# Kernel tuning notes

Hardware: AMD Instinct MI355X
Metric: run time of the kernel (lower is better)

## Reference

```python
import jax, jax.numpy as jnp
import numpy as np

N = 30000      # particles
E = 300000     # directed edges
H = 128        # hidden size
L = 10         # GNN layers
EMB = 16       # particle-type embedding size
T = 5          # velocity history window
NTYPES = 9
RADIUS = 0.05
OUT = 2
NODE_IN = 2 * T + 4 + EMB  # 30


def _mlp_ln(x, W1, b1, W2, b2, W3, b3, g, be):
    # Linear-ReLU-Linear-ReLU-Linear-LayerNorm (matches node/edge encoders and GraphNet blocks)
    h = jax.nn.relu(x @ W1 + b1)
    h = jax.nn.relu(h @ W2 + b2)
    h = h @ W3 + b3
    mu = jnp.mean(h, axis=-1, keepdims=True)
    var = jnp.mean((h - mu) ** 2, axis=-1, keepdims=True)
    return (h - mu) * jax.lax.rsqrt(var + 1e-5) * g + be


def setup_inputs() -> dict:
    key = jax.random.key(0)
    ks = iter(jax.random.split(key, 48))
    nx = lambda: next(ks)
    inp = {}
    inp["vel"] = jax.random.normal(nx(), (N, T, 2), jnp.float32) * 0.01
    inp["pos"] = jax.random.uniform(nx(), (N, 2), dtype=jnp.float32)
    inp["bounds"] = jnp.array([[0.0, 1.0], [0.0, 1.0]], jnp.float32)  # [dim, (lo,hi)]
    inp["tgt_pos"] = jax.random.uniform(nx(), (N, 2), dtype=jnp.float32)
    inp["particle_type"] = jax.random.randint(nx(), (N,), 0, NTYPES, jnp.int32)
    inp["nonk_mask"] = jax.random.randint(nx(), (N,), 0, 2, jnp.int32)
    inp["senders"] = jax.random.randint(nx(), (E,), 0, N, jnp.int32)
    inp["receivers"] = jax.random.randint(nx(), (E,), 0, N, jnp.int32)
    inp["emb"] = jax.random.normal(nx(), (NTYPES, EMB), jnp.float32) * 0.1

    def mlp_p(pre, din, lead=()):
        w = lambda i, o: jax.random.normal(nx(), lead + (i, o), jnp.float32) / np.sqrt(i)
        inp[pre + "_W1"] = w(din, H); inp[pre + "_b1"] = jnp.zeros(lead + (H,), jnp.float32)
        inp[pre + "_W2"] = w(H, H);   inp[pre + "_b2"] = jnp.zeros(lead + (H,), jnp.float32)
        inp[pre + "_W3"] = w(H, H);   inp[pre + "_b3"] = jnp.zeros(lead + (H,), jnp.float32)
        inp[pre + "_g"] = jnp.ones(lead + (H,), jnp.float32)
        inp[pre + "_be"] = jnp.zeros(lead + (H,), jnp.float32)

    mlp_p("ne", NODE_IN)          # node encoder
    mlp_p("ee", 3)                # edge encoder
    mlp_p("ge", 3 * H, (L,))      # per-layer edge-update MLPs
    mlp_p("gn", 2 * H, (L,))      # per-layer node-update MLPs
    inp["de_W1"] = jax.random.normal(nx(), (H, H), jnp.float32) / np.sqrt(H)
    inp["de_b1"] = jnp.zeros((H,), jnp.float32)
    inp["de_W2"] = jax.random.normal(nx(), (H, H), jnp.float32) / np.sqrt(H)
    inp["de_b2"] = jnp.zeros((H,), jnp.float32)
    inp["de_W3"] = jax.random.normal(nx(), (H, OUT), jnp.float32) / np.sqrt(H)
    inp["de_b3"] = jnp.zeros((OUT,), jnp.float32)
    return inp


def reference(vel, pos, bounds, tgt_pos, particle_type, nonk_mask, senders, receivers, emb,
              ne_W1, ne_b1, ne_W2, ne_b2, ne_W3, ne_b3, ne_g, ne_be,
              ee_W1, ee_b1, ee_W2, ee_b2, ee_W3, ee_b3, ee_g, ee_be,
              ge_W1, ge_b1, ge_W2, ge_b2, ge_W3, ge_b3, ge_g, ge_be,
              gn_W1, gn_b1, gn_W2, gn_b2, gn_W3, gn_b3, gn_g, gn_be,
              de_W1, de_b1, de_W2, de_b2, de_W3, de_b3):
    n = pos.shape[0]
    # --- construct node features ---
    vels = vel.reshape(n, -1)                                   # [N, T*2]
    dtw = jnp.concatenate([pos - bounds[:, 0], bounds[:, 1] - pos], axis=1)
    dtw = jnp.clip(dtw / RADIUS, -1.0, 1.0)                     # [N, 4]
    type_emb = emb[particle_type]                               # [N, EMB] gather
    node_attr = jnp.concatenate([vels, dtw, type_emb], axis=1)  # [N, 30]
    # --- construct edge features (senders/receivers precomputed; KD-tree is CPU-side) ---
    dist_vec = (pos[senders] - pos[receivers]) / RADIUS         # [E, 2]
    dist = jnp.linalg.norm(dist_vec, axis=1, keepdims=True)     # [E, 1]
    edge_attr = jnp.concatenate([dist_vec, dist], axis=1)       # [E, 3]
    # --- encode ---
    nodes = _mlp_ln(node_attr, ne_W1, ne_b1, ne_W2, ne_b2, ne_W3, ne_b3, ne_g, ne_be)
    edges = _mlp_ln(edge_attr, ee_W1, ee_b1, ee_W2, ee_b2, ee_W3, ee_b3, ee_g, ee_be)
    # --- process: L message-passing layers with residuals ---
    for l in range(ge_W1.shape[0]):
        e_in = jnp.concatenate([edges, nodes[senders], nodes[receivers]], axis=1)  # [E, 3H]
        edges = edges + _mlp_ln(e_in, ge_W1[l], ge_b1[l], ge_W2[l], ge_b2[l], ge_W3[l], ge_b3[l], ge_g[l], ge_be[l])
        agg = jax.ops.segment_sum(edges, receivers, num_segments=n)               # [N, H] scatter-add
        n_in = jnp.concatenate([nodes, agg], axis=1)                              # [N, 2H]
        nodes = nodes + _mlp_ln(n_in, gn_W1[l], gn_b1[l], gn_W2[l], gn_b2[l], gn_W3[l], gn_b3[l], gn_g[l], gn_be[l])
    # --- decode ---
    h = jax.nn.relu(nodes @ de_W1 + de_b1)
    h = jax.nn.relu(h @ de_W2 + de_b2)
    pred_acc = h @ de_W3 + de_b3                                 # [N, 2]
    # --- Euler integration step (out_size == 2 branch) ---
    pred_pos = pos + vel[:, -1, :] + pred_acc
    pred_pos = jnp.where(nonk_mask[:, None].astype(bool), pred_pos, tgt_pos)
    return pred_acc[:, None, :], pred_pos[:, None, :]
```

## Files before the change

### kernel.cpp

```cpp
#include <hip/hip_runtime.h>
#include <hip/hip_bf16.h>

typedef __hip_bfloat16 bf16;
typedef unsigned short u16;
typedef unsigned int u32;
typedef __attribute__((ext_vector_type(8))) short short8;
typedef __attribute__((ext_vector_type(4))) float f32x4;

#define NPART 30000
#define NEDGE 300000
#define HD 128
#define NLAYER 10
#define NFLOAT_ARRAYS 43
#define NMAT 66

__device__ __forceinline__ bool detect_bf16(const unsigned short* braw) {
    return braw[1] == 0x3F80u;
}

__device__ __forceinline__ u16 f2b(float f) {
    u32 u = __float_as_uint(f);
    u += 0x7FFFu + ((u >> 16) & 1u);
    return (u16)(u >> 16);
}
__device__ __forceinline__ u32 pack2(float a, float b) {
    return (u32)f2b(a) | ((u32)f2b(b) << 16);
}
__device__ __forceinline__ float b2flo(u32 u) { return __uint_as_float(u << 16); }
__device__ __forceinline__ float b2fhi(u32 u) { return __uint_as_float(u & 0xFFFF0000u); }

struct ConvArgs {
    const void* src[NFLOAT_ARRAYS];
    int n[NFLOAT_ARRAYS];
    int off[NFLOAT_ARRAYS];
};

__global__ __launch_bounds__(256)
void k_convert(ConvArgs a, float* __restrict__ dst, const unsigned short* __restrict__ braw)
{
    const bool isb = detect_bf16(braw);
    const int aid = blockIdx.y;
    const int n = a.n[aid];
    float* o = dst + a.off[aid];
    const int stride = gridDim.x * 256;
    int i = blockIdx.x * 256 + threadIdx.x;
    if (isb) {
        const unsigned short* s = (const unsigned short*)a.src[aid];
        for (; i < n; i += stride) {
            const unsigned int u = ((unsigned int)s[i]) << 16;
            o[i] = __uint_as_float(u);
        }
    } else {
        const float* s = (const float*)a.src[aid];
        for (; i < n; i += stride) o[i] = s[i];
    }
}

__global__ __launch_bounds__(256)
void k_hist(const int* __restrict__ rcv, int* __restrict__ counts)
{
    const int e = blockIdx.x * 256 + threadIdx.x;
    if (e < NEDGE) atomicAdd(&counts[rcv[e]], 1);
}

__global__ __launch_bounds__(1024)
void k_scan(const int* __restrict__ counts, int* __restrict__ row_ptr, int* __restrict__ cursor)
{
    __shared__ int part[1024];
    const int t = threadIdx.x;
    const int base = t * 32;
    int local[32];
    int s = 0;
#pragma unroll
    for (int k = 0; k < 32; k++) {
        const int idx = base + k;
        const int v = (idx < NPART) ? counts[idx] : 0;
        local[k] = s;
        s += v;
    }
    part[t] = s;
    __syncthreads();
    for (int off = 1; off < 1024; off <<= 1) {
        const int v = (t >= off) ? part[t - off] : 0;
        __syncthreads();
        part[t] += v;
        __syncthreads();
    }
    const int excl = (t == 0) ? 0 : part[t - 1];
#pragma unroll
    for (int k = 0; k < 32; k++) {
        const int idx = base + k;
        if (idx < NPART) {
            const int rp = excl + local[k];
            row_ptr[idx] = rp;
            cursor[idx] = rp;
        }
    }
    if (t == 0) row_ptr[NPART] = NEDGE;
}

__global__ __launch_bounds__(256)
void k_scatter(const int* __restrict__ snd, const int* __restrict__ rcv,
               int* __restrict__ cursor, int* __restrict__ snd_s, int* __restrict__ rcv_s)
{
    const int e = blockIdx.x * 256 + threadIdx.x;
    if (e < NEDGE) {
        const int r = rcv[e];
        const int p = atomicAdd(&cursor[r], 1);
        snd_s[p] = snd[e];
        rcv_s[p] = r;
    }
}

struct PackArgs {
    int src_off[NMAT];
    int dst_off[NMAT];
    int K[NMAT];
    int nks[NMAT];
};

__global__ __launch_bounds__(256)
void k_pack(const float* __restrict__ cw, u16* __restrict__ wpk, PackArgs pa)
{
    const int mid = blockIdx.y;
    const int nks = pa.nks[mid];
    const int total = nks * 4096;
    const int d = blockIdx.x * 256 + threadIdx.x;
    if (d >= total) return;
    const int j = d & 7, l = (d >> 3) & 63, t = d >> 9;
    const int ks = t % nks, mt = t / nks;
    const int hid = mt * 16 + (l & 15);
    const int k = ks * 32 + (l >> 4) * 8 + j;
    const float v = (k < pa.K[mid]) ? cw[pa.src_off[mid] + k * HD + hid] : 0.0f;
    wpk[pa.dst_off[mid] + d] = f2b(v);
}

template<int NKS, int XROW>
__device__ __forceinline__ void gemm16(const u16* __restrict__ Wp,
                                       const float* __restrict__ Bias,
                                       const u16* __restrict__ x,
                                       f32x4 acc[4][2],
                                       const int wm, const int wn,
                                       const int l15, const int lg, const int lane)
{
#pragma unroll
    for (int mt = 0; mt < 4; mt++) {
        const f32x4 bv = *(const f32x4*)(Bias + wm * 64 + mt * 16 + lg * 4);
        acc[mt][0] = bv;
        acc[mt][1] = bv;
    }
    const u16* xr0 = x + (wn * 32 + l15) * XROW + lg * 8;
    const u16* xr1 = xr0 + 16 * XROW;
    const u16* wp = Wp + (wm * 4 * NKS) * 512 + lane * 8;
#pragma unroll
    for (int ks = 0; ks < NKS; ks++) {
        const short8 b0 = *(const short8*)(xr0 + ks * 32);
        const short8 b1 = *(const short8*)(xr1 + ks * 32);
#pragma unroll
        for (int mt = 0; mt < 4; mt++) {
            const short8 a = *(const short8*)(wp + (mt * NKS + ks) * 512);
            acc[mt][0] = __builtin_amdgcn_mfma_f32_16x16x32_bf16(a, b0, acc[mt][0], 0, 0, 0);
            acc[mt][1] = __builtin_amdgcn_mfma_f32_16x16x32_bf16(a, b1, acc[mt][1], 0, 0, 0);
        }
    }
}

__device__ __forceinline__ void store_h(u16* __restrict__ h, const f32x4 acc[4][2],
                                        const int wm, const int wn, const int l15, const int lg)
{
#pragma unroll
    for (int nt = 0; nt < 2; nt++) {
        const int e = wn * 32 + nt * 16 + l15;
#pragma unroll
        for (int mt = 0; mt < 4; mt++) {
            const int hid = wm * 64 + mt * 16 + lg * 4;
            const f32x4 v = acc[mt][nt];
            const u32 lo = pack2(fmaxf(v[0], 0.0f), fmaxf(v[1], 0.0f));
            const u32 hi = pack2(fmaxf(v[2], 0.0f), fmaxf(v[3], 0.0f));
            *(uint2*)(h + e * 136 + hid) = make_uint2(lo, hi);
        }
    }
}

template<int NKS1, int XROW>
__device__ __forceinline__ void mlp_mfma(const u16* __restrict__ xs,
    u16* __restrict__ h1, u16* __restrict__ h2,
    float (*red)[2][2][16][2],
    const u16* __restrict__ W1p, const float* __restrict__ B1,
    const u16* __restrict__ W2p, const float* __restrict__ B2,
    const u16* __restrict__ W3p, const float* __restrict__ B3,
    const float* __restrict__ g, const float* __restrict__ be,
    float outv[4][2][4],
    const int wm, const int wn, const int l15, const int lg, const int lane)
{
    f32x4 acc[4][2];
    gemm16<NKS1, XROW>(W1p, B1, xs, acc, wm, wn, l15, lg, lane);
    __syncthreads();
    store_h(h1, acc, wm, wn, l15, lg);
    __syncthreads();
    gemm16<4, 136>(W2p, B2, h1, acc, wm, wn, l15, lg, lane);
    store_h(h2, acc, wm, wn, l15, lg);
    __syncthreads();
    gemm16<4, 136>(W3p, B3, h2, acc, wm, wn, l15, lg, lane);
    float ps[2], pss[2];
#pragma unroll
    for (int nt = 0; nt < 2; nt++) {
        float s = 0.0f, ss = 0.0f;
#pragma unroll
        for (int mt = 0; mt < 4; mt++) {
#pragma unroll
            for (int r = 0; r < 4; r++) {
                const float v = acc[mt][nt][r];
                s += v; ss += v * v;
            }
        }
        s += __shfl_xor(s, 16); ss += __shfl_xor(ss, 16);
        s += __shfl_xor(s, 32); ss += __shfl_xor(ss, 32);
        ps[nt] = s; pss[nt] = ss;
    }
    if (lane < 16) {
#pragma unroll
        for (int nt = 0; nt < 2; nt++) {
            red[wm][wn][nt][l15][0] = ps[nt];
            red[wm][wn][nt][l15][1] = pss[nt];
        }
    }
    __syncthreads();
#pragma unroll
    for (int nt = 0; nt < 2; nt++) {
        const float S  = red[0][wn][nt][l15][0] + red[1][wn][nt][l15][0];
        const float SS = red[0][wn][nt][l15][1] + red[1][wn][nt][l15][1];
        const float mu  = S * (1.0f / 128.0f);
        const float var = SS * (1.0f / 128.0f) - mu * mu;
        const float inv = rsqrtf(var + 1e-5f);
#pragma unroll
        for (int mt = 0; mt < 4; mt++) {
            const int hid = wm * 64 + mt * 16 + lg * 4;
            const f32x4 gv  = *(const f32x4*)(g + hid);
            const f32x4 bev = *(const f32x4*)(be + hid);
#pragma unroll
            for (int r = 0; r < 4; r++)
                outv[mt][nt][r] = (acc[mt][nt][r] - mu) * inv * gv[r] + bev[r];
        }
    }
}

__device__ __forceinline__ float nfeat(int i, int k,
    const float* __restrict__ vel, const float* __restrict__ pos,
    const float* __restrict__ bounds, const int* __restrict__ ptype,
    const float* __restrict__ emb)
{
    if (k < 10) return vel[i * 10 + k];
    if (k < 14) {
        const int q = k - 10;
        float sub;
        if (q < 2) sub = pos[i * 2 + q] - bounds[q * 2 + 0];
        else       sub = bounds[(q - 2) * 2 + 1] - pos[i * 2 + (q - 2)];
        const float dv = sub * 20.0f;
        return fminf(fmaxf(dv, -1.0f), 1.0f);
    }
    if (k < 30) return emb[ptype[i] * 16 + (k - 14)];
    return 0.0f;
}

__global__ __launch_bounds__(256)
void k_node_enc_m(const float* __restrict__ vel, const float* __restrict__ pos,
                  const float* __restrict__ bounds, const int* __restrict__ ptype,
                  const float* __restrict__ emb,
                  const u16* __restrict__ W1p, const float* __restrict__ B1,
                  const u16* __restrict__ W2p, const float* __restrict__ B2,
                  const u16* __restrict__ W3p, const float* __restrict__ B3,
                  const float* __restrict__ g, const float* __restrict__ be,
                  float* __restrict__ nodes, u16* __restrict__ nodes_bf)
{
    __shared__ __align__(16) u16 lds[17408];
    __shared__ float red[2][2][2][16][2];
    const int tid = threadIdx.x;
    const int i0 = blockIdx.x * 64;
    for (int idx = tid; idx < 1024; idx += 256) {
        const int m = idx >> 4, kk = idx & 15;
        const int i = i0 + m;
        float f0 = 0.0f, f1 = 0.0f;
        if (i < NPART) {
            f0 = nfeat(i, kk * 2 + 0, vel, pos, bounds, ptype, emb);
            f1 = nfeat(i, kk * 2 + 1, vel, pos, bounds, ptype, emb);
        }
        *(u32*)(lds + m * 40 + kk * 2) = pack2(f0, f1);
    }
    __syncthreads();
    const int lane = tid & 63, wv = tid >> 6;
    const int wm = wv >> 1, wn = wv & 1, l15 = lane & 15, lg = lane >> 4;
    float outv[4][2][4];
    mlp_mfma<1, 40>(lds, lds, lds + 8704, red, W1p, B1, W2p, B2, W3p, B3, g, be,
                    outv, wm, wn, l15, lg, lane);
#pragma unroll
    for (int nt = 0; nt < 2; nt++) {
        const int i = i0 + wn * 32 + nt * 16 + l15;
        if (i < NPART) {
#pragma unroll
            for (int mt = 0; mt < 4; mt++) {
                const int hid = wm * 64 + mt * 16 + lg * 4;
                const float4 v = make_float4(outv[mt][nt][0], outv[mt][nt][1],
                                             outv[mt][nt][2], outv[mt][nt][3]);
                *(float4*)(nodes + (size_t)i * HD + hid) = v;
                *(uint2*)(nodes_bf + (size_t)i * HD + hid) =
                    make_uint2(pack2(v.x, v.y), pack2(v.z, v.w));
            }
        }
    }
}

__global__ __launch_bounds__(256)
void k_edge_enc_m(const float* __restrict__ pos, const int* __restrict__ snd_s,
                  const int* __restrict__ rcv_s,
                  const u16* __restrict__ W1p, const float* __restrict__ B1,
                  const u16* __restrict__ W2p, const float* __restrict__ B2,
                  const u16* __restrict__ W3p, const float* __restrict__ B3,
                  const float* __restrict__ g, const float* __restrict__ be,
                  u16* __restrict__ edges_bf)
{
    __shared__ __align__(16) u16 lds[17408];
    __shared__ float red[2][2][2][16][2];
    const int tid = threadIdx.x;
    const int e0 = blockIdx.x * 64;
    for (int idx = tid; idx < 1024; idx += 256) {
        const int m = idx >> 4, kk = idx & 15;
        const int e = min(e0 + m, NEDGE - 1);
        u32 w = 0;
        if (kk < 2) {
            const int s = snd_s[e], r = rcv_s[e];
            const float dx = (pos[s * 2 + 0] - pos[r * 2 + 0]) * 20.0f;
            const float dy = (pos[s * 2 + 1] - pos[r * 2 + 1]) * 20.0f;
            if (kk == 0) w = pack2(dx, dy);
            else         w = pack2(sqrtf(dx * dx + dy * dy), 0.0f);
        }
        *(u32*)(lds + m * 40 + kk * 2) = w;
    }
    __syncthreads();
    const int lane = tid & 63, wv = tid >> 6;
    const int wm = wv >> 1, wn = wv & 1, l15 = lane & 15, lg = lane >> 4;
    float outv[4][2][4];
    mlp_mfma<1, 40>(lds, lds, lds + 8704, red, W1p, B1, W2p, B2, W3p, B3, g, be,
                    outv, wm, wn, l15, lg, lane);
#pragma unroll
    for (int nt = 0; nt < 2; nt++) {
        const int e = e0 + wn * 32 + nt * 16 + l15;
        if (e < NEDGE) {
#pragma unroll
            for (int mt = 0; mt < 4; mt++) {
                const int hid = wm * 64 + mt * 16 + lg * 4;
                *(uint2*)(edges_bf + (size_t)e * HD + hid) =
                    make_uint2(pack2(outv[mt][nt][0], outv[mt][nt][1]),
                               pack2(outv[mt][nt][2], outv[mt][nt][3]));
            }
        }
    }
}

__device__ __forceinline__ void egemm_seg32(const u16* __restrict__ Wp,
                                            const u16* __restrict__ x,
                                            f32x4 acc[2][2], const int ks0,
                                            const int wm,
                                            const int l15, const int lg, const int lane)
{
    const u16* xr0 = x + l15 * 136 + lg * 8;
    const u16* xr1 = xr0 + 16 * 136;
#pragma unroll
    for (int ks = 0; ks < 4; ks++) {
        const short8 b0 = *(const short8*)(xr0 + ks * 32);
        const short8 b1 = *(const short8*)(xr1 + ks * 32);
#pragma unroll
        for (int mt = 0; mt < 2; mt++) {
            const short8 a = *(const short8*)(Wp + (((wm * 2 + mt) * 12 + ks0 + ks) * 64 + lane) * 8);
            acc[mt][0] = __builtin_amdgcn_mfma_f32_16x16x32_bf16(a, b0, acc[mt][0], 0, 0, 0);
            acc[mt][1] = __builtin_amdgcn_mfma_f32_16x16x32_bf16(a, b1, acc[mt][1], 0, 0, 0);
        }
    }
}

__device__ __forceinline__ void egemm_h32(const u16* __restrict__ Wp,
                                          const float* __restrict__ Bias,
                                          const u16* __restrict__ x,
                                          f32x4 acc[2][2],
                                          const int wm,
                                          const int l15, const int lg, const int lane)
{
#pragma unroll
    for (int mt = 0; mt < 2; mt++) {
        const f32x4 bv = *(const f32x4*)(Bias + wm * 32 + mt * 16 + lg * 4);
        acc[mt][0] = bv;
        acc[mt][1] = bv;
    }
    const u16* xr0 = x + l15 * 136 + lg * 8;
    const u16* xr1 = xr0 + 16 * 136;
#pragma unroll
    for (int ks = 0; ks < 4; ks++) {
        const short8 b0 = *(const short8*)(xr0 + ks * 32);
        const short8 b1 = *(const short8*)(xr1 + ks * 32);
#pragma unroll
        for (int mt = 0; mt < 2; mt++) {
            const short8 a = *(const short8*)(Wp + (((wm * 2 + mt) * 4 + ks) * 64 + lane) * 8);
            acc[mt][0] = __builtin_amdgcn_mfma_f32_16x16x32_bf16(a, b0, acc[mt][0], 0, 0, 0);
            acc[mt][1] = __builtin_amdgcn_mfma_f32_16x16x32_bf16(a, b1, acc[mt][1], 0, 0, 0);
        }
    }
}

__device__ __forceinline__ void estore_h32(u16* __restrict__ h, const f32x4 acc[2][2],
                                           const int wm, const int l15, const int lg)
{
#pragma unroll
    for (int nt = 0; nt < 2; nt++) {
        const int row = nt * 16 + l15;
#pragma unroll
        for (int mt = 0; mt < 2; mt++) {
            const int hid = wm * 32 + mt * 16 + lg * 4;
            const f32x4 v = acc[mt][nt];
            const u32 lo = pack2(fmaxf(v[0], 0.0f), fmaxf(v[1], 0.0f));
            const u32 hi = pack2(fmaxf(v[2], 0.0f), fmaxf(v[3], 0.0f));
            *(uint2*)(h + row * 136 + hid) = make_uint2(lo, hi);
        }
    }
}

__global__ __launch_bounds__(256, 8)
void k_edge_layer_m(const u16* __restrict__ nodes_bf, u16* __restrict__ edges_bf,
                    float* __restrict__ agg, float* __restrict__ bnd,
                    const int* __restrict__ snd_s, const int* __restrict__ rcv_s,
                    const u16* __restrict__ W1p, const float* __restrict__ B1,
                    const u16* __restrict__ W2p, const float* __restrict__ B2,
                    const u16* __restrict__ W3p, const float* __restrict__ B3,
                    const float* __restrict__ g, const float* __restrict__ be)
{
    __shared__ __align__(16) u16 sb[2 * 4352];
    __shared__ float red[4][2][16][2];
    __shared__ int rblk[34];
    u16* b0 = sb;
    u16* b1 = sb + 4352;
    float* fout = (float*)sb;

    const int tid = threadIdx.x;
    const int e0 = blockIdx.x * 32;
    const int lane = tid & 63, wm = tid >> 6;
    const int l15 = lane & 15, lg = lane >> 4;

    if (tid < 32)       rblk[tid] = rcv_s[e0 + tid];
    else if (tid == 32) rblk[32] = (e0 > 0) ? rcv_s[e0 - 1] : -2;
    else if (tid == 33) rblk[33] = (e0 + 32 < NEDGE) ? rcv_s[e0 + 32] : -2;

    uint4 e_old[2];
#pragma unroll
    for (int t = 0; t < 2; t++) {
        const int idx = tid + t * 256;
        const int m = idx >> 4, q = idx & 15;
        e_old[t] = *(const uint4*)(edges_bf + (size_t)(e0 + m) * HD + q * 8);
        *(uint4*)(b0 + m * 136 + q * 8) = e_old[t];
    }
    uint4 st[2];
#pragma unroll
    for (int t = 0; t < 2; t++) {
        const int idx = tid + t * 256;
        const int m = idx >> 4, q = idx & 15;
        st[t] = *(const uint4*)(nodes_bf + (size_t)snd_s[e0 + m] * HD + q * 8);
    }
    __syncthreads();

    f32x4 acc[2][2];
#pragma unroll
    for (int mt = 0; mt < 2; mt++) {
        const f32x4 bv = *(const f32x4*)(B1 + wm * 32 + mt * 16 + lg * 4);
        acc[mt][0] = bv;
        acc[mt][1] = bv;
    }
    __builtin_amdgcn_s_setprio(1);
    egemm_seg32(W1p, b0, acc, 0, wm, l15, lg, lane);
    __builtin_amdgcn_s_setprio(0);
#pragma unroll
    for (int t = 0; t < 2; t++) {
        const int idx = tid + t * 256;
        const int m = idx >> 4, q = idx & 15;
        *(uint4*)(b1 + m * 136 + q * 8) = st[t];
    }
#pragma unroll
    for (int t = 0; t < 2; t++) {
        const int idx = tid + t * 256;
        const int m = idx >> 4, q = idx & 15;
        st[t] = *(const uint4*)(nodes_bf + (size_t)rcv_s[e0 + m] * HD + q * 8);
    }
    __syncthreads();

    __builtin_amdgcn_s_setprio(1);
    egemm_seg32(W1p, b1, acc, 4, wm, l15, lg, lane);
    __builtin_amdgcn_s_setprio(0);
#pragma unroll
    for (int t = 0; t < 2; t++) {
        const int idx = tid + t * 256;
        const int m = idx >> 4, q = idx & 15;
        *(uint4*)(b0 + m * 136 + q * 8) = st[t];
    }
    __syncthreads();

    __builtin_amdgcn_s_setprio(1);
    egemm_seg32(W1p, b0, acc, 8, wm, l15, lg, lane);
    __builtin_amdgcn_s_setprio(0);
    estore_h32(b1, acc, wm, l15, lg);
    __syncthreads();

    __builtin_amdgcn_s_setprio(1);
    egemm_h32(W2p, B2, b1, acc, wm, l15, lg, lane);
    __builtin_amdgcn_s_setprio(0);
    estore_h32(b0, acc, wm, l15, lg);
    __syncthreads();

    __builtin_amdgcn_s_setprio(1);
    egemm_h32(W3p, B3, b0, acc, wm, l15, lg, lane);
    __builtin_amdgcn_s_setprio(0);

    float ps[2], pss[2];
#pragma unroll
    for (int nt = 0; nt < 2; nt++) {
        float s = 0.0f, ss = 0.0f;
#pragma unroll
        for (int mt = 0; mt < 2; mt++) {
#pragma unroll
            for (int r = 0; r < 4; r++) {
                const float v = acc[mt][nt][r];
                s += v; ss += v * v;
            }
        }
        s += __shfl_xor(s, 16); ss += __shfl_xor(ss, 16);
        s += __shfl_xor(s, 32); ss += __shfl_xor(ss, 32);
        ps[nt] = s; pss[nt] = ss;
    }
    if (lane < 16) {
#pragma unroll
        for (int nt = 0; nt < 2; nt++) {
            red[wm][nt][l15][0] = ps[nt];
            red[wm][nt][l15][1] = pss[nt];
        }
    }
    __syncthreads();

#pragma unroll
    for (int nt = 0; nt < 2; nt++) {
        const float S  = red[0][nt][l15][0] + red[1][nt][l15][0]
                       + red[2][nt][l15][0] + red[3][nt][l15][0];
        const float SS = red[0][nt][l15][1] + red[1][nt][l15][1]
                       + red[2][nt][l15][1] + red[3][nt][l15][1];
        const float mu  = S * (1.0f / 128.0f);
        const float var = SS * (1.0f / 128.0f) - mu * mu;
        const float inv = rsqrtf(var + 1e-5f);
        const int row = nt * 16 + l15;
#pragma unroll
        for (int mt = 0; mt < 2; mt++) {
            const int hid = wm * 32 + mt * 16 + lg * 4;
            const f32x4 gv  = *(const f32x4*)(g + hid);
            const f32x4 bev = *(const f32x4*)(be + hid);
            f32x4 o;
#pragma unroll
            for (int r = 0; r < 4; r++)
                o[r] = (acc[mt][nt][r] - mu) * inv * gv[r] + bev[r];
            *(f32x4*)(fout + row * 132 + hid) = o;
        }
    }
    __syncthreads();

#pragma unroll
    for (int t = 0; t < 2; t++) {
        const int idx = tid + t * 256;
        const int m = idx >> 4, q = idx & 15;
        float4 lo = *(const float4*)(fout + m * 132 + q * 8);
        float4 hi = *(const float4*)(fout + m * 132 + q * 8 + 4);
        const uint4 o = e_old[t];
        lo.x += b2flo(o.x); lo.y += b2fhi(o.x);
        lo.z += b2flo(o.y); lo.w += b2fhi(o.y);
        hi.x += b2flo(o.z); hi.y += b2fhi(o.z);
        hi.z += b2flo(o.w); hi.w += b2fhi(o.w);
        *(float4*)(fout + m * 132 + q * 8) = lo;
        *(float4*)(fout + m * 132 + q * 8 + 4) = hi;
        *(uint4*)(edges_bf + (size_t)(e0 + m) * HD + q * 8) =
            make_uint4(pack2(lo.x, lo.y), pack2(lo.z, lo.w),
                       pack2(hi.x, hi.y), pack2(hi.z, hi.w));
    }
    __syncthreads();

    const int c = tid & 31;
    for (int ms = (tid >> 5); ms < 32; ms += 8) {
        const int rs = rblk[ms];
        if (ms > 0 && rblk[ms - 1] == rs) continue;
        int me = ms + 1;
        while (me < 32 && rblk[me] == rs) me++;
        float4 s = make_float4(0.0f, 0.0f, 0.0f, 0.0f);
        for (int m = ms; m < me; m++) {
            const float4 v = *(const float4*)(fout + m * 132 + c * 4);
            s.x += v.x; s.y += v.y; s.z += v.z; s.w += v.w;
        }
        const bool extb = (ms == 0 && rblk[32] == rs);
        const bool extf = (me == 32 && rblk[33] == rs);
        float* ap;
        if (!extb && !extf) ap = agg + (size_t)rs * HD + c * 4;
        else ap = bnd + ((size_t)blockIdx.x * 2 + (extb ? 0 : 1)) * HD + c * 4;
        *(float4*)ap = s;
    }
}

__global__ __launch_bounds__(256)
void k_node_layer_m(float* __restrict__ nodes, u16* __restrict__ nodes_bf,
                    const float* __restrict__ agg, const float* __restrict__ bnd,
                    const int* __restrict__ row_ptr,
                    const u16* __restrict__ W1p, const float* __restrict__ B1,
                    const u16* __restrict__ W2p, const float* __restrict__ B2,
                    const u16* __restrict__ W3p, const float* __restrict__ B3,
                    const float* __restrict__ g, const float* __restrict__ be)
{
    __shared__ __align__(16) u16 lds[17408];
    __shared__ float red[2][2][2][16][2];
    __shared__ int rp[65];
    const int tid = threadIdx.x;
    const int i0 = blockIdx.x * 64;
    if (tid < 65) rp[tid] = row_ptr[min(i0 + tid, NPART)];
    __syncthreads();
    for (int idx = tid; idx < 1024; idx += 256) {
        const int m = idx >> 4, q = idx & 15;
        const int i = min(i0 + m, NPART - 1);
        const float* src = nodes + (size_t)i * HD + q * 8;
        const float4 a = *(const float4*)(src);
        const float4 b = *(const float4*)(src + 4);
        *(uint4*)(lds + m * 264 + q * 8) =
            make_uint4(pack2(a.x, a.y), pack2(a.z, a.w), pack2(b.x, b.y), pack2(b.z, b.w));
    }
    for (int idx = tid; idx < 1024; idx += 256) {
        const int m = idx >> 4, q = idx & 15;
        const int i = i0 + m;
        float4 a = make_float4(0.0f, 0.0f, 0.0f, 0.0f);
        float4 b = make_float4(0.0f, 0.0f, 0.0f, 0.0f);
        if (i < NPART) {
            const int p0 = rp[m], p1 = rp[m + 1];
            if (p1 > p0) {
                const int b0 = p0 >> 5, b1 = (p1 - 1) >> 5;
                if (b0 == b1) {
                    const float* src = agg + (size_t)i * HD + q * 8;
                    a = *(const float4*)(src);
                    b = *(const float4*)(src + 4);
                } else {
                    const float* s1 = bnd + ((size_t)b0 * 2 + 1) * HD + q * 8;
                    a = *(const float4*)(s1);
                    b = *(const float4*)(s1 + 4);
                    for (int bb = b0 + 1; bb <= b1; bb++) {
                        const float* s0 = bnd + ((size_t)bb * 2 + 0) * HD + q * 8;
                        const float4 xa = *(const float4*)(s0);
                        const float4 xb = *(const float4*)(s0 + 4);
                        a.x += xa.x; a.y += xa.y; a.z += xa.z; a.w += xa.w;
                        b.x += xb.x; b.y += xb.y; b.z += xb.z; b.w += xb.w;
                    }
                }
            }
        }
        *(uint4*)(lds + m * 264 + 128 + q * 8) =
            make_uint4(pack2(a.x, a.y), pack2(a.z, a.w), pack2(b.x, b.y), pack2(b.z, b.w));
    }
    __syncthreads();
    const int lane = tid & 63, wv = tid >> 6;
    const int wm = wv >> 1, wn = wv & 1, l15 = lane & 15, lg = lane >> 4;
    float outv[4][2][4];
    mlp_mfma<8, 264>(lds, lds, lds + 8704, red, W1p, B1, W2p, B2, W3p, B3, g, be,
                     outv, wm, wn, l15, lg, lane);
#pragma unroll
    for (int nt = 0; nt < 2; nt++) {
        const int i = i0 + wn * 32 + nt * 16 + l15;
        if (i < NPART) {
            float* np = nodes + (size_t)i * HD;
#pragma unroll
            for (int mt = 0; mt < 4; mt++) {
                const int hid = wm * 64 + mt * 16 + lg * 4;
                const float4 old = *(const float4*)(np + hid);
                const float4 nv = make_float4(old.x + outv[mt][nt][0],
                                              old.y + outv[mt][nt][1],
                                              old.z + outv[mt][nt][2],
                                              old.w + outv[mt][nt][3]);
                *(float4*)(np + hid) = nv;
                *(uint2*)(nodes_bf + (size_t)i * HD + hid) =
                    make_uint2(pack2(nv.x, nv.y), pack2(nv.z, nv.w));
            }
        }
    }
}

template<int K, int S>
__device__ __forceinline__ void gemv(const float* __restrict__ in,
                                     const float* __restrict__ W,
                                     const float* __restrict__ B,
                                     float acc[8])
{
    const int j = threadIdx.x;
    const float bb = B[j];
#pragma unroll
    for (int m = 0; m < 8; m++) acc[m] = bb;
    constexpr int K4 = (K / 4) * 4;
    for (int k = 0; k < K4; k += 4) {
        const float w0 = W[(k + 0) * HD + j];
        const float w1 = W[(k + 1) * HD + j];
        const float w2 = W[(k + 2) * HD + j];
        const float w3 = W[(k + 3) * HD + j];
#pragma unroll
        for (int m = 0; m < 8; m++) {
            const float4 x = *(const float4*)(in + m * S + k);
            float a = acc[m];
            a = fmaf(x.x, w0, a);
            a = fmaf(x.y, w1, a);
            a = fmaf(x.z, w2, a);
            a = fmaf(x.w, w3, a);
            acc[m] = a;
        }
    }
#pragma unroll
    for (int k = K4; k < K; k++) {
        const float w = W[k * HD + j];
#pragma unroll
        for (int m = 0; m < 8; m++) acc[m] = fmaf(in[m * S + k], w, acc[m]);
    }
}

__global__ __launch_bounds__(128)
void k_decoder(const float* __restrict__ nodes,
               const float* W1, const float* B1, const float* W2, const float* B2,
               const float* W3, const float* B3,
               const float* __restrict__ vel, const float* __restrict__ pos,
               const float* __restrict__ tgt, const int* __restrict__ nonk,
               const unsigned short* __restrict__ braw, void* __restrict__ d_out)
{
    __shared__ __align__(16) float xs[8 * HD];
    __shared__ __align__(16) float h1[8 * HD];
    __shared__ __align__(16) float h2[8 * HD];
    const int j = threadIdx.x;
    const int i0 = blockIdx.x * 8;
    float acc[8];
#pragma unroll
    for (int m = 0; m < 8; m++) xs[m * HD + j] = nodes[(i0 + m) * HD + j];
    __syncthreads();
    gemv<HD, HD>(xs, W1, B1, acc);
#pragma unroll
    for (int m = 0; m < 8; m++) h1[m * HD + j] = fmaxf(acc[m], 0.0f);
    __syncthreads();
    gemv<HD, HD>(h1, W2, B2, acc);
#pragma unroll
    for (int m = 0; m < 8; m++) h2[m * HD + j] = fmaxf(acc[m], 0.0f);
    __syncthreads();
    if (j < 16) {
        const int m = j >> 1, d = j & 1, i = i0 + m;
        float a = B3[d];
        for (int k = 0; k < HD; k++) a = fmaf(h2[m * HD + k], W3[k * 2 + d], a);
        float pp = pos[i * 2 + d] + vel[i * 10 + 8 + d] + a;
        if (nonk[i] == 0) pp = tgt[i * 2 + d];
        if (detect_bf16(braw)) {
            bf16* o = (bf16*)d_out;
            o[i * 2 + d] = __float2bfloat16(a);
            o[2 * NPART + i * 2 + d] = __float2bfloat16(pp);
        } else {
            float* o = (float*)d_out;
            o[i * 2 + d] = a;
            o[2 * NPART + i * 2 + d] = pp;
        }
    }
}

extern "C" void kernel_launch(void* const* d_in, const int* in_sizes, int n_in,
                              void* d_out, int out_size, void* d_ws, size_t ws_size,
                              hipStream_t stream)
{
    const int* ptype = (const int*)d_in[4];
    const int* nonk  = (const int*)d_in[5];
    const int* snd   = (const int*)d_in[6];
    const int* rcv   = (const int*)d_in[7];
    const unsigned short* braw = (const unsigned short*)d_in[2];

    int fmap[NFLOAT_ARRAYS];
    {
        int c = 0;
        fmap[c++] = 0; fmap[c++] = 1; fmap[c++] = 2; fmap[c++] = 3; fmap[c++] = 8;
        for (int i = 9; i <= 46; i++) fmap[c++] = i;
    }
    ConvArgs ca;
    const float* fp[47];
    float* cw = (float*)d_ws;
    int off = 0;
    for (int i = 0; i < NFLOAT_ARRAYS; i++) {
        ca.src[i] = d_in[fmap[i]];
        ca.n[i]   = in_sizes[fmap[i]];
        ca.off[i] = off;
        fp[fmap[i]] = cw + off;
        off += in_sizes[fmap[i]];
    }
    const int EB32 = NEDGE / 32;
    float* nodes = cw + ((off + 3) & ~3);
    float* agg   = nodes + (size_t)NPART * HD;
    float* bnd   = agg + (size_t)NPART * HD;
    u16* edges_bf = (u16*)(bnd + (size_t)EB32 * 2 * HD);
    u16* nodes_bf = edges_bf + (size_t)NEDGE * HD;
    u16* wpk = nodes_bf + (size_t)NPART * HD;

    PackArgs pa;
    int dst = 0, c = 0;
    int pk[NMAT];
    auto addm = [&](long srcoff, int K) {
        const int nk = (K + 31) / 32;
        pa.src_off[c] = (int)srcoff;
        pa.K[c] = K;
        pa.nks[c] = nk;
        pa.dst_off[c] = dst;
        pk[c] = dst;
        dst += nk * 4096;
        c++;
    };
    addm(fp[9]  - cw, 30);  addm(fp[11] - cw, 128); addm(fp[13] - cw, 128);
    addm(fp[17] - cw, 3);   addm(fp[19] - cw, 128); addm(fp[21] - cw, 128);
    for (int l = 0; l < NLAYER; l++) {
        addm(fp[25] - cw + (long)l * 384 * HD, 384);
        addm(fp[27] - cw + (long)l * HD * HD, 128);
        addm(fp[29] - cw + (long)l * HD * HD, 128);
    }
    for (int l = 0; l < NLAYER; l++) {
        addm(fp[33] - cw + (long)l * 256 * HD, 256);
        addm(fp[35] - cw + (long)l * HD * HD, 128);
        addm(fp[37] - cw + (long)l * HD * HD, 128);
    }

    int* ip = (int*)(wpk + ((dst + 7) & ~7));
    int* row_ptr = ip;            ip += NPART + 8;
    int* cursor  = ip;            ip += NPART;
    int* counts  = ip;            ip += NPART;
    int* snd_s   = ip;            ip += NEDGE;
    int* rcv_s   = ip;

    const int EBL = (NEDGE + 255) / 256;

    k_convert<<<dim3(64, NFLOAT_ARRAYS), 256, 0, stream>>>(ca, cw, braw);
    hipMemsetAsync(counts, 0, (size_t)NPART * sizeof(int), stream);
    k_hist<<<EBL, 256, 0, stream>>>(rcv, counts);
    k_scan<<<1, 1024, 0, stream>>>(counts, row_ptr, cursor);
    k_scatter<<<EBL, 256, 0, stream>>>(snd, rcv, cursor, snd_s, rcv_s);
    k_pack<<<dim3(192, NMAT), 256, 0, stream>>>(cw, wpk, pa);

    const int NB = (NPART + 63) / 64;
    const int EB = (NEDGE + 63) / 64;

    k_node_enc_m<<<NB, 256, 0, stream>>>(fp[0], fp[1], fp[2], ptype, fp[8],
        wpk + pk[0], fp[10], wpk + pk[1], fp[12], wpk + pk[2], fp[14],
        fp[15], fp[16], nodes, nodes_bf);
    k_edge_enc_m<<<EB, 256, 0, stream>>>(fp[1], snd_s, rcv_s,
        wpk + pk[3], fp[18], wpk + pk[4], fp[20], wpk + pk[5], fp[22],
        fp[23], fp[24], edges_bf);

    for (int l = 0; l < NLAYER; l++) {
        k_edge_layer_m<<<EB32, 256, 0, stream>>>(nodes_bf, edges_bf, agg, bnd, snd_s, rcv_s,
            wpk + pk[6 + 3 * l],  fp[26] + (size_t)l * HD,
            wpk + pk[7 + 3 * l],  fp[28] + (size_t)l * HD,
            wpk + pk[8 + 3 * l],  fp[30] + (size_t)l * HD,
            fp[31] + (size_t)l * HD, fp[32] + (size_t)l * HD);
        k_node_layer_m<<<NB, 256, 0, stream>>>(nodes, nodes_bf, agg, bnd, row_ptr,
            wpk + pk[36 + 3 * l], fp[34] + (size_t)l * HD,
            wpk + pk[37 + 3 * l], fp[36] + (size_t)l * HD,
            wpk + pk[38 + 3 * l], fp[38] + (size_t)l * HD,
            fp[39] + (size_t)l * HD, fp[40] + (size_t)l * HD);
    }

    k_decoder<<<NPART / 8, 128, 0, stream>>>(nodes,
        fp[41], fp[42], fp[43], fp[44], fp[45], fp[46],
        fp[0], fp[1], fp[3], nonk, braw, d_out);
}
```

Measured before the change: 2.207 ms.

## Drop fp32 node copy, keep nodes only in bf16, add nontemporal streaming accesses

Removes the fp32 `nodes` array. The node encoder, node layers and decoder now read and write only the bf16 node state, and the residual add is done from bf16. Separately, the per-edge `edges_bf` and `agg`/`bnd` traffic now uses nontemporal loads and stores so single-use streaming data does not pollute the caches. Together these cut node-state memory traffic, but the residual now accumulates in bf16 across layers, which lowers precision and could drift the outputs.

```diff
diff --git a/kernel.cpp b/kernel.cpp
--- a/kernel.cpp
+++ b/kernel.cpp
@@ -6,6 +6,7 @@
 typedef unsigned int u32;
 typedef __attribute__((ext_vector_type(8))) short short8;
 typedef __attribute__((ext_vector_type(4))) float f32x4;
+typedef __attribute__((ext_vector_type(4))) unsigned int u32x4;
 
 #define NPART 30000
 #define NEDGE 300000
@@ -28,6 +29,19 @@
 }
 __device__ __forceinline__ float b2flo(u32 u) { return __uint_as_float(u << 16); }
 __device__ __forceinline__ float b2fhi(u32 u) { return __uint_as_float(u & 0xFFFF0000u); }
+
+__device__ __forceinline__ u32x4 ntl4(const u16* p) {
+    return __builtin_nontemporal_load((const u32x4*)p);
+}
+__device__ __forceinline__ void nts4(const u32x4 v, u16* p) {
+    __builtin_nontemporal_store(v, (u32x4*)p);
+}
+__device__ __forceinline__ f32x4 ntlf4(const float* p) {
+    return __builtin_nontemporal_load((const f32x4*)p);
+}
+__device__ __forceinline__ void ntsf4(const f32x4 v, float* p) {
+    __builtin_nontemporal_store(v, (f32x4*)p);
+}
 
 struct ConvArgs {
     const void* src[NFLOAT_ARRAYS];
@@ -271,7 +285,7 @@
                   const u16* __restrict__ W2p, const float* __restrict__ B2,
                   const u16* __restrict__ W3p, const float* __restrict__ B3,
                   const float* __restrict__ g, const float* __restrict__ be,
-                  float* __restrict__ nodes, u16* __restrict__ nodes_bf)
+                  u16* __restrict__ nodes_bf)
 {
     __shared__ __align__(16) u16 lds[17408];
     __shared__ float red[2][2][2][16][2];
@@ -300,11 +314,9 @@
 #pragma unroll
             for (int mt = 0; mt < 4; mt++) {
                 const int hid = wm * 64 + mt * 16 + lg * 4;
-                const float4 v = make_float4(outv[mt][nt][0], outv[mt][nt][1],
-                                             outv[mt][nt][2], outv[mt][nt][3]);
-                *(float4*)(nodes + (size_t)i * HD + hid) = v;
                 *(uint2*)(nodes_bf + (size_t)i * HD + hid) =
-                    make_uint2(pack2(v.x, v.y), pack2(v.z, v.w));
+                    make_uint2(pack2(outv[mt][nt][0], outv[mt][nt][1]),
+                               pack2(outv[mt][nt][2], outv[mt][nt][3]));
             }
         }
     }
@@ -448,20 +460,20 @@
     else if (tid == 32) rblk[32] = (e0 > 0) ? rcv_s[e0 - 1] : -2;
     else if (tid == 33) rblk[33] = (e0 + 32 < NEDGE) ? rcv_s[e0 + 32] : -2;
 
-    uint4 e_old[2];
+    u32x4 e_old[2];
 #pragma unroll
     for (int t = 0; t < 2; t++) {
         const int idx = tid + t * 256;
         const int m = idx >> 4, q = idx & 15;
-        e_old[t] = *(const uint4*)(edges_bf + (size_t)(e0 + m) * HD + q * 8);
-        *(uint4*)(b0 + m * 136 + q * 8) = e_old[t];
-    }
-    uint4 st[2];
+        e_old[t] = ntl4(edges_bf + (size_t)(e0 + m) * HD + q * 8);
+        *(u32x4*)(b0 + m * 136 + q * 8) = e_old[t];
+    }
+    u32x4 st[2];
 #pragma unroll
     for (int t = 0; t < 2; t++) {
         const int idx = tid + t * 256;
         const int m = idx >> 4, q = idx & 15;
-        st[t] = *(const uint4*)(nodes_bf + (size_t)snd_s[e0 + m] * HD + q * 8);
+        st[t] = *(const u32x4*)(nodes_bf + (size_t)snd_s[e0 + m] * HD + q * 8);
     }
     __syncthreads();
 
@@ -479,13 +491,13 @@
     for (int t = 0; t < 2; t++) {
         const int idx = tid + t * 256;
         const int m = idx >> 4, q = idx & 15;
-        *(uint4*)(b1 + m * 136 + q * 8) = st[t];
+        *(u32x4*)(b1 + m * 136 + q * 8) = st[t];
     }
 #pragma unroll
     for (int t = 0; t < 2; t++) {
         const int idx = tid + t * 256;
         const int m = idx >> 4, q = idx & 15;
-        st[t] = *(const uint4*)(nodes_bf + (size_t)rcv_s[e0 + m] * HD + q * 8);
+        st[t] = *(const u32x4*)(nodes_bf + (size_t)rcv_s[e0 + m] * HD + q * 8);
     }
     __syncthreads();
 
@@ -496,7 +508,7 @@
     for (int t = 0; t < 2; t++) {
         const int idx = tid + t * 256;
         const int m = idx >> 4, q = idx & 15;
-        *(uint4*)(b0 + m * 136 + q * 8) = st[t];
+        *(u32x4*)(b0 + m * 136 + q * 8) = st[t];
     }
     __syncthreads();
 
@@ -571,16 +583,17 @@
         const int m = idx >> 4, q = idx & 15;
         float4 lo = *(const float4*)(fout + m * 132 + q * 8);
         float4 hi = *(const float4*)(fout + m * 132 + q * 8 + 4);
-        const uint4 o = e_old[t];
+        const u32x4 o = e_old[t];
         lo.x += b2flo(o.x); lo.y += b2fhi(o.x);
         lo.z += b2flo(o.y); lo.w += b2fhi(o.y);
         hi.x += b2flo(o.z); hi.y += b2fhi(o.z);
         hi.z += b2flo(o.w); hi.w += b2fhi(o.w);
         *(float4*)(fout + m * 132 + q * 8) = lo;
         *(float4*)(fout + m * 132 + q * 8 + 4) = hi;
-        *(uint4*)(edges_bf + (size_t)(e0 + m) * HD + q * 8) =
-            make_uint4(pack2(lo.x, lo.y), pack2(lo.z, lo.w),
-                       pack2(hi.x, hi.y), pack2(hi.z, hi.w));
+        u32x4 nv;
+        nv.x = pack2(lo.x, lo.y); nv.y = pack2(lo.z, lo.w);
+        nv.z = pack2(hi.x, hi.y); nv.w = pack2(hi.z, hi.w);
+        nts4(nv, edges_bf + (size_t)(e0 + m) * HD + q * 8);
     }
     __syncthreads();
 
@@ -590,7 +603,7 @@
         if (ms > 0 && rblk[ms - 1] == rs) continue;
         int me = ms + 1;
         while (me < 32 && rblk[me] == rs) me++;
-        float4 s = make_float4(0.0f, 0.0f, 0.0f, 0.0f);
+        f32x4 s = {0.0f, 0.0f, 0.0f, 0.0f};
         for (int m = ms; m < me; m++) {
             const float4 v = *(const float4*)(fout + m * 132 + c * 4);
             s.x += v.x; s.y += v.y; s.z += v.z; s.w += v.w;
@@ -600,12 +613,12 @@
         float* ap;
         if (!extb && !extf) ap = agg + (size_t)rs * HD + c * 4;
         else ap = bnd + ((size_t)blockIdx.x * 2 + (extb ? 0 : 1)) * HD + c * 4;
-        *(float4*)ap = s;
+        ntsf4(s, ap);
     }
 }
 
 __global__ __launch_bounds__(256)
-void k_node_layer_m(float* __restrict__ nodes, u16* __restrict__ nodes_bf,
+void k_node_layer_m(u16* __restrict__ nodes_bf,
                     const float* __restrict__ agg, const float* __restrict__ bnd,
                     const int* __restrict__ row_ptr,
                     const u16* __restrict__ W1p, const float* __restrict__ B1,
@@ -623,41 +636,38 @@
     for (int idx = tid; idx < 1024; idx += 256) {
         const int m = idx >> 4, q = idx & 15;
         const int i = min(i0 + m, NPART - 1);
-        const float* src = nodes + (size_t)i * HD + q * 8;
-        const float4 a = *(const float4*)(src);
-        const float4 b = *(const float4*)(src + 4);
-        *(uint4*)(lds + m * 264 + q * 8) =
-            make_uint4(pack2(a.x, a.y), pack2(a.z, a.w), pack2(b.x, b.y), pack2(b.z, b.w));
+        *(u32x4*)(lds + m * 264 + q * 8) =
+            *(const u32x4*)(nodes_bf + (size_t)i * HD + q * 8);
     }
     for (int idx = tid; idx < 1024; idx += 256) {
         const int m = idx >> 4, q = idx & 15;
         const int i = i0 + m;
-        float4 a = make_float4(0.0f, 0.0f, 0.0f, 0.0f);
-        float4 b = make_float4(0.0f, 0.0f, 0.0f, 0.0f);
+        f32x4 a = {0.0f, 0.0f, 0.0f, 0.0f};
+        f32x4 b = {0.0f, 0.0f, 0.0f, 0.0f};
         if (i < NPART) {
             const int p0 = rp[m], p1 = rp[m + 1];
             if (p1 > p0) {
                 const int b0 = p0 >> 5, b1 = (p1 - 1) >> 5;
                 if (b0 == b1) {
                     const float* src = agg + (size_t)i * HD + q * 8;
-                    a = *(const float4*)(src);
-                    b = *(const float4*)(src + 4);
+                    a = ntlf4(src);
+                    b = ntlf4(src + 4);
                 } else {
                     const float* s1 = bnd + ((size_t)b0 * 2 + 1) * HD + q * 8;
-                    a = *(const float4*)(s1);
-                    b = *(const float4*)(s1 + 4);
+                    a = ntlf4(s1);
+                    b = ntlf4(s1 + 4);
                     for (int bb = b0 + 1; bb <= b1; bb++) {
                         const float* s0 = bnd + ((size_t)bb * 2 + 0) * HD + q * 8;
-                        const float4 xa = *(const float4*)(s0);
-                        const float4 xb = *(const float4*)(s0 + 4);
-                        a.x += xa.x; a.y += xa.y; a.z += xa.z; a.w += xa.w;
-                        b.x += xb.x; b.y += xb.y; b.z += xb.z; b.w += xb.w;
+                        const f32x4 xa = ntlf4(s0);
+                        const f32x4 xb = ntlf4(s0 + 4);
+                        a += xa;
+                        b += xb;
                     }
                 }
             }
         }
-        *(uint4*)(lds + m * 264 + 128 + q * 8) =
-            make_uint4(pack2(a.x, a.y), pack2(a.z, a.w), pack2(b.x, b.y), pack2(b.z, b.w));
+        *(u32x4*)(lds + m * 264 + 128 + q * 8) = (u32x4){
+            pack2(a.x, a.y), pack2(a.z, a.w), pack2(b.x, b.y), pack2(b.z, b.w)};
     }
     __syncthreads();
     const int lane = tid & 63, wv = tid >> 6;
@@ -669,18 +679,17 @@
     for (int nt = 0; nt < 2; nt++) {
         const int i = i0 + wn * 32 + nt * 16 + l15;
         if (i < NPART) {
-            float* np = nodes + (size_t)i * HD;
+            u16* np = nodes_bf + (size_t)i * HD;
 #pragma unroll
             for (int mt = 0; mt < 4; mt++) {
                 const int hid = wm * 64 + mt * 16 + lg * 4;
-                const float4 old = *(const float4*)(np + hid);
-                const float4 nv = make_float4(old.x + outv[mt][nt][0],
-                                              old.y + outv[mt][nt][1],
-                                              old.z + outv[mt][nt][2],
-                                              old.w + outv[mt][nt][3]);
-                *(float4*)(np + hid) = nv;
-                *(uint2*)(nodes_bf + (size_t)i * HD + hid) =
-                    make_uint2(pack2(nv.x, nv.y), pack2(nv.z, nv.w));
+                const uint2 ob = *(const uint2*)(np + hid);
+                float4 nv;
+                nv.x = b2flo(ob.x) + outv[mt][nt][0];
+                nv.y = b2fhi(ob.x) + outv[mt][nt][1];
+                nv.z = b2flo(ob.y) + outv[mt][nt][2];
+                nv.w = b2fhi(ob.y) + outv[mt][nt][3];
+                *(uint2*)(np + hid) = make_uint2(pack2(nv.x, nv.y), pack2(nv.z, nv.w));
             }
         }
     }
@@ -722,7 +731,7 @@
 }
 
 __global__ __launch_bounds__(128)
-void k_decoder(const float* __restrict__ nodes,
+void k_decoder(const u16* __restrict__ nodes_bf,
                const float* W1, const float* B1, const float* W2, const float* B2,
                const float* W3, const float* B3,
                const float* __restrict__ vel, const float* __restrict__ pos,
@@ -735,8 +744,12 @@
     const int j = threadIdx.x;
     const int i0 = blockIdx.x * 8;
     float acc[8];
-#pragma unroll
-    for (int m = 0; m < 8; m++) xs[m * HD + j] = nodes[(i0 + m) * HD + j];
+    for (int idx = j; idx < 512; idx += 128) {
+        const int m = idx >> 6, q = idx & 63;
+        const u32 w = *(const u32*)(nodes_bf + (size_t)(i0 + m) * HD + q * 2);
+        xs[m * HD + q * 2]     = b2flo(w);
+        xs[m * HD + q * 2 + 1] = b2fhi(w);
+    }
     __syncthreads();
     gemv<HD, HD>(xs, W1, B1, acc);
 #pragma unroll
@@ -792,8 +805,7 @@
         off += in_sizes[fmap[i]];
     }
     const int EB32 = NEDGE / 32;
-    float* nodes = cw + ((off + 3) & ~3);
-    float* agg   = nodes + (size_t)NPART * HD;
+    float* agg   = cw + ((off + 3) & ~3);
     float* bnd   = agg + (size_t)NPART * HD;
     u16* edges_bf = (u16*)(bnd + (size_t)EB32 * 2 * HD);
     u16* nodes_bf = edges_bf + (size_t)NEDGE * HD;
@@ -846,7 +858,7 @@
 
     k_node_enc_m<<<NB, 256, 0, stream>>>(fp[0], fp[1], fp[2], ptype, fp[8],
         wpk + pk[0], fp[10], wpk + pk[1], fp[12], wpk + pk[2], fp[14],
-        fp[15], fp[16], nodes, nodes_bf);
+        fp[15], fp[16], nodes_bf);
     k_edge_enc_m<<<EB, 256, 0, stream>>>(fp[1], snd_s, rcv_s,
         wpk + pk[3], fp[18], wpk + pk[4], fp[20], wpk + pk[5], fp[22],
         fp[23], fp[24], edges_bf);
@@ -857,14 +869,14 @@
             wpk + pk[7 + 3 * l],  fp[28] + (size_t)l * HD,
             wpk + pk[8 + 3 * l],  fp[30] + (size_t)l * HD,
             fp[31] + (size_t)l * HD, fp[32] + (size_t)l * HD);
-        k_node_layer_m<<<NB, 256, 0, stream>>>(nodes, nodes_bf, agg, bnd, row_ptr,
+        k_node_layer_m<<<NB, 256, 0, stream>>>(nodes_bf, agg, bnd, row_ptr,
             wpk + pk[36 + 3 * l], fp[34] + (size_t)l * HD,
             wpk + pk[37 + 3 * l], fp[36] + (size_t)l * HD,
             wpk + pk[38 + 3 * l], fp[38] + (size_t)l * HD,
             fp[39] + (size_t)l * HD, fp[40] + (size_t)l * HD);
     }
 
-    k_decoder<<<NPART / 8, 128, 0, stream>>>(nodes,
+    k_decoder<<<NPART / 8, 128, 0, stream>>>(nodes_bf,
         fp[41], fp[42], fp[43], fp[44], fp[45], fp[46],
         fp[0], fp[1], fp[3], nonk, braw, d_out);
 }
```

Result: faster. 1.835 ms (-16.8%).
